# Kernel tuning notes

Measured on AMD Instinct MI355X. Metric: run time of the kernel, lower is better.

Reference implementation:

```python
import jax, jax.numpy as jnp
import numpy as np

B = 512
N_ENT = 100000
N_REL = 64
D = 200          # embed_dim
D1 = 10          # embed_shape (emb_dim1)
D2 = 20          # embed_dim // embed_shape (emb_dim2)
K = 3            # kernel_size
C = 32           # out_channels
FC_IN = C * (2 * D1 - K + 1) * (D2 - K + 1)  # 32*18*18 = 10368
EPS = 1e-5       # BatchNorm eps
LS = 0.1         # label_smoothing
LAM = 1e-5       # kg_l2_loss_lambda


def setup_inputs() -> dict:
    key = jax.random.key(0)
    ks = jax.random.split(key, 8)
    return dict(
        entity_w=jax.random.normal(ks[0], (N_ENT, D), jnp.float32) * 0.1,
        relation_w=jax.random.normal(ks[1], (N_REL, D), jnp.float32) * 0.1,
        conv_w=jax.random.normal(ks[2], (C, 1, K, K), jnp.float32) * 0.1,
        conv_b=jnp.zeros((C,), jnp.float32),
        fc_w=jax.random.normal(ks[3], (D, FC_IN), jnp.float32) * 0.02,
        fc_b=jnp.zeros((D,), jnp.float32),
        b=jnp.zeros((N_ENT,), jnp.float32),
        bn0_g=jnp.ones((1,), jnp.float32), bn0_b=jnp.zeros((1,), jnp.float32),
        bn1_g=jnp.ones((C,), jnp.float32), bn1_b=jnp.zeros((C,), jnp.float32),
        bn2_g=jnp.ones((D,), jnp.float32), bn2_b=jnp.zeros((D,), jnp.float32),
        h=jax.random.randint(ks[4], (B,), 0, N_ENT),
        r=jax.random.randint(ks[5], (B,), 0, N_REL),
        pos_t=jax.random.randint(ks[6], (B,), 0, N_ENT),
    )


def _bn(x, g, b, axes, shape):
    # training-mode batchnorm (batch statistics), biased variance as in torch
    m = jnp.mean(x, axes, keepdims=True)
    v = jnp.var(x, axes, keepdims=True)
    return (x - m) * jax.lax.rsqrt(v + EPS) * g.reshape(shape) + b.reshape(shape)


def _l2_mean(x):
    # torch: mean(sum(x**2, dim=1) / 2)
    return jnp.mean(jnp.sum(x * x, axis=1) / 2.0)


def reference(entity_w, relation_w, conv_w, conv_b, fc_w, fc_b, b,
              bn0_g, bn0_b, bn1_g, bn1_b, bn2_g, bn2_b, h, r, pos_t):
    h_e = entity_w[h].reshape(B, 1, D1, D2)
    r_e = relation_w[r].reshape(B, 1, D1, D2)
    x = jnp.concatenate([h_e, r_e], axis=2)           # [B,1,2*D1,D2]
    x = _bn(x, bn0_g, bn0_b, (0, 2, 3), (1, 1, 1, 1))
    x = jax.lax.conv_general_dilated(
        x, conv_w, (1, 1), 'VALID',
        dimension_numbers=('NCHW', 'OIHW', 'NCHW')) + conv_b.reshape(1, C, 1, 1)
    x = _bn(x, bn1_g, bn1_b, (0, 2, 3), (1, C, 1, 1))
    x = jax.nn.relu(x).reshape(B, -1)                 # [B, FC_IN]
    x = x @ fc_w.T + fc_b                             # [B, D]
    x = _bn(x, bn2_g, bn2_b, (0,), (1, D))
    x = jax.nn.leaky_relu(x)                          # slope 0.01 = torch default
    scores = x @ entity_w.T + b                       # [B, N_ENT]
    # BCEWithLogits with smoothed label y = (1-LS)*onehot(pos_t) + 1/N_ENT,
    # loss = mean(softplus(s) - s*y); one-hot never materialized.
    sp_sum = jnp.sum(jax.nn.softplus(scores))
    xy_sum = jnp.sum(scores) / N_ENT + (1.0 - LS) * jnp.sum(
        scores[jnp.arange(B), pos_t])
    kg_loss = (sp_sum - xy_sum) / (B * N_ENT)
    l2 = _l2_mean(h_e) + _l2_mean(r_e) + _l2_mean(conv_w) + _l2_mean(fc_w)
    return kg_loss + LAM * l2
```

## Files before the change

kernel.cpp:

```cpp
#include <hip/hip_runtime.h>
#include <math.h>

#define NB_B 512
#define NE 100000
#define NE_PAD 100032
#define DD 200
#define CC 32
#define FCIN 10368
#define HW 324
#define BNEPS 1e-5f
#define KP 224

#define ENT2_BLKS 3126
#define FCW_BLKS 1013
#define GATH_OFF2 (ENT2_BLKS + FCW_BLKS)

typedef __attribute__((ext_vector_type(8))) short short8;
typedef __attribute__((ext_vector_type(4))) float floatx4;


static __device__ __forceinline__ float blk_reduce(float v, volatile float* sbuf) {
  for (int o = 32; o > 0; o >>= 1) v += __shfl_down(v, o, 64);
  int lane = threadIdx.x & 63, wid = threadIdx.x >> 6;
  if (lane == 0) sbuf[wid] = v;
  __syncthreads();
  float r = 0.f;
  int nw = (blockDim.x + 63) >> 6;
  if ((int)threadIdx.x < nw) r = sbuf[threadIdx.x];
  if (threadIdx.x < 64) {
    for (int o = 32; o > 0; o >>= 1) r += __shfl_down(r, o, 64);
  }
  __syncthreads();
  return r;
}

static __device__ __forceinline__ unsigned short f32_to_bf16(float f) {
  unsigned int u = __float_as_uint(f);
  u += 0x7fffu + ((u >> 16) & 1u);
  return (unsigned short)(u >> 16);
}
static __device__ __forceinline__ float bf16_to_f32(unsigned short b) {
  return __uint_as_float(((unsigned int)b) << 16);
}

__global__ __launch_bounds__(256) void k_cvt(const float* __restrict__ ent,
                                             unsigned short* __restrict__ entb,
                                             const float* __restrict__ fcw,
                                             unsigned short* __restrict__ fcwb,
                                             const float* __restrict__ rel,
                                             const int* __restrict__ h,
                                             const int* __restrict__ r,
                                             float* __restrict__ x0,
                                             double* dacc) {
  __shared__ float xs[6432];
  int t = threadIdx.x;
  if (blockIdx.x < ENT2_BLKS) {
    int tile = blockIdx.x;
    for (int g = t; g < 1600; g += 256) {
      int rr = g / 50, c4 = g - rr * 50;
      int row = tile * 32 + rr;
      float4 u = {0.f, 0.f, 0.f, 0.f};
      if (row < NE) u = *(const float4*)(ent + (long)row * DD + c4 * 4);
      float* p = &xs[rr * 201 + c4 * 4];
      p[0] = u.x; p[1] = u.y; p[2] = u.z; p[3] = u.w;
    }
    __syncthreads();
    unsigned short* dst = entb + (long)tile * 7168;
    for (int g = t; g < 896; g += 256) {
      int c = g >> 5, rr = g & 31;
      short8 o = (short8){0, 0, 0, 0, 0, 0, 0, 0};
      if (c < 25) {
        const float* p = &xs[rr * 201 + c * 8];
        o[0] = (short)f32_to_bf16(p[0]); o[1] = (short)f32_to_bf16(p[1]);
        o[2] = (short)f32_to_bf16(p[2]); o[3] = (short)f32_to_bf16(p[3]);
        o[4] = (short)f32_to_bf16(p[4]); o[5] = (short)f32_to_bf16(p[5]);
        o[6] = (short)f32_to_bf16(p[6]); o[7] = (short)f32_to_bf16(p[7]);
      }
      *(short8*)(dst + g * 8) = o;
    }
  } else if (blockIdx.x < GATH_OFF2) {
    int g = (blockIdx.x - ENT2_BLKS) * 256 + t;
    float sq = 0.f;
    if (g < 259200) {
      const float4* s = (const float4*)(fcw + (long)g * 8);
      float4 u = s[0], v = s[1];
      sq = u.x*u.x + u.y*u.y + u.z*u.z + u.w*u.w
         + v.x*v.x + v.y*v.y + v.z*v.z + v.w*v.w;
      ushort4 o0, o1;
      o0.x = f32_to_bf16(u.x); o0.y = f32_to_bf16(u.y);
      o0.z = f32_to_bf16(u.z); o0.w = f32_to_bf16(u.w);
      o1.x = f32_to_bf16(v.x); o1.y = f32_to_bf16(v.y);
      o1.z = f32_to_bf16(v.z); o1.w = f32_to_bf16(v.w);
      ushort4* d = (ushort4*)(fcwb + (long)g * 8);
      d[0] = o0; d[1] = o1;
    }
    float tq = blk_reduce(sq, xs);
    if (t == 0) atomicAdd(&dacc[67], (double)tq);
  } else {
    int b = blockIdx.x - GATH_OFF2;
    int hi = h[b], ri = r[b];
    float s = 0.f, sq = 0.f;
    for (int i = t; i < 400; i += 256) {
      float v = (i < 200) ? ent[(long)hi * DD + i] : rel[(long)ri * DD + (i - 200)];
      x0[b * 400 + i] = v;
      s += v; sq += v * v;
    }
    float ts = blk_reduce(s, xs);
    float tq = blk_reduce(sq, xs);
    if (t == 0) {
      atomicAdd(&dacc[0], (double)ts);
      atomicAdd(&dacc[1], (double)tq);
    }
  }
}

__global__ __launch_bounds__(256) void k_conv(const float* __restrict__ x0,
                       const float* __restrict__ convw, const float* __restrict__ convb,
                       const float* __restrict__ g0, const float* __restrict__ b0,
                       unsigned short* __restrict__ yb, double* dacc) {
  __shared__ float xs[400], wsm[288], cbs[32], ssum[32], ssq[32];
  __shared__ float a0s, s0s;
  int b = blockIdx.x, t = threadIdx.x;
  for (int i = t; i < 400; i += 256) xs[i] = x0[b * 400 + i];
  for (int i = t; i < 288; i += 256) wsm[i] = convw[i];
  if (t < 32) cbs[t] = convb[t];
  if (t == 0) {
    double m = dacc[0] / 204800.0;
    double v = dacc[1] / 204800.0 - m * m;
    float a = g0[0] * rsqrtf((float)v + BNEPS);
    a0s = a; s0s = b0[0] - (float)m * a;
  }
  __syncthreads();
  float a0 = a0s, s0 = s0s;
  for (int i = t; i < 400; i += 256) xs[i] = a0 * xs[i] + s0;
  __syncthreads();
  int c = t >> 3, sub = t & 7;
  const float* w = &wsm[c * 9];
  float cb = cbs[c];
  float s = 0.f, sq = 0.f;
  for (int e = sub; e < HW; e += 8) {
    int oh = e / 18, ow = e - oh * 18;
    const float* xp = &xs[oh * 20 + ow];
    float acc = cb
       + xp[0] * w[0] + xp[1] * w[1] + xp[2] * w[2]
       + xp[20] * w[3] + xp[21] * w[4] + xp[22] * w[5]
       + xp[40] * w[6] + xp[41] * w[7] + xp[42] * w[8];
    yb[(long)b * FCIN + c * HW + e] = f32_to_bf16(acc);
    s += acc; sq += acc * acc;
  }
  s += __shfl_xor(s, 1, 64); sq += __shfl_xor(sq, 1, 64);
  s += __shfl_xor(s, 2, 64); sq += __shfl_xor(sq, 2, 64);
  s += __shfl_xor(s, 4, 64); sq += __shfl_xor(sq, 4, 64);
  if (sub == 0) { ssum[c] = s; ssq[c] = sq; }
  __syncthreads();
  if (t < 32) {
    atomicAdd(&dacc[2 + t], (double)ssum[t]);
    atomicAdd(&dacc[34 + t], (double)ssq[t]);
  }
}

__global__ __launch_bounds__(256) void k_prep(unsigned short* __restrict__ yb,
                                              const float* __restrict__ g1,
                                              const float* __restrict__ b1,
                                              const double* __restrict__ dacc) {
  __shared__ float a1s[32], sh1s[32];
  int t = threadIdx.x;
  if (t < 32) {
    double cnt = 512.0 * 324.0;
    double m = dacc[2 + t] / cnt, v = dacc[34 + t] / cnt - m * m;
    float a = g1[t] * rsqrtf((float)v + BNEPS);
    a1s[t] = a; sh1s[t] = b1[t] - (float)m * a;
  }
  __syncthreads();
  int g = blockIdx.x * 256 + t;
  int row = g / 1296;
  int c8 = (g - row * 1296) * 8;
  unsigned short* p = yb + (long)row * FCIN + c8;
  ushort4 v0 = ((ushort4*)p)[0], v1 = ((ushort4*)p)[1];
  unsigned short e[8] = {v0.x, v0.y, v0.z, v0.w, v1.x, v1.y, v1.z, v1.w};
#pragma unroll
  for (int j = 0; j < 8; j++) {
    int c = (c8 + j) / HW;
    float f = a1s[c] * bf16_to_f32(e[j]) + sh1s[c];
    e[j] = f32_to_bf16(fmaxf(f, 0.f));
  }
  v0.x = e[0]; v0.y = e[1]; v0.z = e[2]; v0.w = e[3];
  v1.x = e[4]; v1.y = e[5]; v1.z = e[6]; v1.w = e[7];
  ((ushort4*)p)[0] = v0; ((ushort4*)p)[1] = v1;
}

__global__ __launch_bounds__(64) void k_fc3(const unsigned short* __restrict__ yb,
                                            const unsigned short* __restrict__ fcwb,
                                            float* __restrict__ Cp) {
  int wid = blockIdx.x;
  int ks = wid >> 5, rem = wid & 31;
  int mt = rem >> 2, nt = rem & 3;
  int m0 = mt * 64, n0 = nt * 64;
  int lane = threadIdx.x;
  int quad = lane >> 4, lr = lane & 15;
  long kbeg = (long)ks * 864;

  const unsigned short* arow[4];
  const unsigned short* brow[4];
#pragma unroll
  for (int mi = 0; mi < 4; mi++)
    arow[mi] = yb + (long)(m0 + mi * 16 + lr) * FCIN + kbeg + quad * 8;
#pragma unroll
  for (int ni = 0; ni < 4; ni++) {
    int d = n0 + ni * 16 + lr;
    if (d > DD - 1) d = DD - 1;
    brow[ni] = fcwb + (long)d * FCIN + kbeg + quad * 8;
  }

  floatx4 acc[4][4];
#pragma unroll
  for (int i = 0; i < 4; i++)
#pragma unroll
    for (int j = 0; j < 4; j++) acc[i][j] = (floatx4){0.f, 0.f, 0.f, 0.f};

  short8 sA[3][4], sB[3][4];
#pragma unroll
  for (int c = 0; c < 3; c++) {
#pragma unroll
    for (int mi = 0; mi < 4; mi++) sA[c][mi] = *(const short8*)(arow[mi] + c * 32);
#pragma unroll
    for (int ni = 0; ni < 4; ni++) sB[c][ni] = *(const short8*)(brow[ni] + c * 32);
  }
  for (int c3 = 0; c3 < 9; c3++) {
    int cc = c3 * 3;
#pragma unroll
    for (int j = 0; j < 3; j++) {
#pragma unroll
      for (int ni = 0; ni < 4; ni++)
#pragma unroll
        for (int mi = 0; mi < 4; mi++)
          acc[mi][ni] = __builtin_amdgcn_mfma_f32_16x16x32_bf16(sA[j][mi], sB[j][ni], acc[mi][ni], 0, 0, 0);
      int nxt = cc + j + 3;
      if (nxt < 27) {
#pragma unroll
        for (int mi = 0; mi < 4; mi++) sA[j][mi] = *(const short8*)(arow[mi] + nxt * 32);
#pragma unroll
        for (int ni = 0; ni < 4; ni++) sB[j][ni] = *(const short8*)(brow[ni] + nxt * 32);
      }
    }
  }

  float* out = Cp + (long)ks * (NB_B * DD);
#pragma unroll
  for (int ni = 0; ni < 4; ni++) {
    int d = n0 + ni * 16 + lr;
    if (d < DD) {
#pragma unroll
      for (int mi = 0; mi < 4; mi++) {
        int mbase = m0 + mi * 16 + quad * 4;
#pragma unroll
        for (int rg = 0; rg < 4; rg++)
          out[(mbase + rg) * DD + d] = acc[mi][ni][rg];
      }
    }
  }
}

__global__ void k_fcbn(const float* __restrict__ Cp, const float* __restrict__ fcb,
                       const float* __restrict__ g2, const float* __restrict__ b2,
                       float* __restrict__ Cfc, float* __restrict__ a2,
                       float* __restrict__ b2c) {
  int d = blockIdx.x, lane = threadIdx.x;
  float fb = fcb[d];
  float s = 0.f, sq = 0.f;
  for (int b = lane; b < NB_B; b += 64) {
    float v = 0.f;
#pragma unroll
    for (int p = 0; p < 12; p++) v += Cp[(long)p * (NB_B * DD) + b * DD + d];
    Cfc[b * DD + d] = v;
    float w = v + fb;
    s += w; sq += w * w;
  }
  for (int o = 32; o > 0; o >>= 1) { s += __shfl_down(s, o, 64); sq += __shfl_down(sq, o, 64); }
  if (lane == 0) {
    float m = s / 512.f, v = sq / 512.f - m * m;
    float a = g2[d] * rsqrtf(v + BNEPS);
    a2[d] = a; b2c[d] = b2[d] - m * a;
  }
}

__global__ __launch_bounds__(256) void k_xfinal(const float* __restrict__ Cfc,
                         const float* __restrict__ fcb,
                         const float* __restrict__ a2, const float* __restrict__ b2c,
                         const float* __restrict__ ent, const float* __restrict__ bias,
                         const int* __restrict__ pos,
                         float* __restrict__ xf, unsigned short* __restrict__ xfb,
                         double* dacc) {
  __shared__ float xs[224];
  __shared__ float sbuf[8];
  int b = blockIdx.x, t = threadIdx.x;
  if (t < KP) {
    float xv = 0.f;
    if (t < DD) {
      float v = Cfc[b * DD + t] + fcb[t];
      xv = a2[t] * v + b2c[t];
      xv = xv >= 0.f ? xv : 0.01f * xv;
      xf[b * DD + t] = xv;
    }
    xfb[b * KP + t] = f32_to_bf16(xv);
    xs[t] = xv;
  }
  __syncthreads();
  int e = pos[b];
  float s = (t < DD) ? xs[t] * ent[(long)e * DD + t] : 0.f;
  float ts = blk_reduce(s, sbuf);
  if (t == 0) atomicAdd(&dacc[70], (double)(ts + bias[e]));
}

static __device__ __forceinline__ void sc_compute10(
    const unsigned short* __restrict__ buf, const float (&bv)[2],
    const short8 (&af)[2][7], int quad, int lr, float& sp, float& ss) {
#pragma unroll
  for (int ni = 0; ni < 2; ni++) {
    float b1v = bv[ni];
    floatx4 acc0 = (floatx4){0.f, 0.f, 0.f, 0.f};
    floatx4 acc1 = (floatx4){0.f, 0.f, 0.f, 0.f};
#pragma unroll
    for (int kc = 0; kc < 7; kc++) {
      int c = kc * 4 + quad;
      short8 bsv = *(const short8*)(buf + c * 256 + (ni * 16 + lr) * 8);
      acc0 = __builtin_amdgcn_mfma_f32_16x16x32_bf16(af[0][kc], bsv, acc0, 0, 0, 0);
      acc1 = __builtin_amdgcn_mfma_f32_16x16x32_bf16(af[1][kc], bsv, acc1, 0, 0, 0);
    }
#pragma unroll
    for (int rg2 = 0; rg2 < 4; rg2++) {
      float s1 = acc0[rg2] + b1v;
      ss += s1;
      float m1 = s1 * 1.4426950408889634f;
      float e2 = __builtin_amdgcn_exp2f(-__builtin_fabsf(m1));
      sp += fmaxf(m1, 0.f) + __builtin_amdgcn_logf(1.f + e2);
    }
#pragma unroll
    for (int rg2 = 0; rg2 < 4; rg2++) {
      float s1 = acc1[rg2] + b1v;
      ss += s1;
      float m1 = s1 * 1.4426950408889634f;
      float e2 = __builtin_amdgcn_exp2f(-__builtin_fabsf(m1));
      sp += fmaxf(m1, 0.f) + __builtin_amdgcn_logf(1.f + e2);
    }
  }
}

__global__ __launch_bounds__(512) void k_scores11(
    const unsigned short* __restrict__ entb,
    const unsigned short* __restrict__ xfb,
    const float* __restrict__ bias, double* dacc) {
  __shared__ unsigned short Bs[2][7168];
  __shared__ float sbuf[8];
  int t = threadIdx.x;
  int wv = t >> 6, lane = t & 63;
  int quad = lane >> 4, lr = lane & 15;
  int b = blockIdx.x;
  int rh = b & 1;
  int chunk = b >> 1;
  int nt = (chunk < 54) ? 7 : 6;
  int t0 = chunk * 6 + (chunk < 54 ? chunk : 54);

  short8 af[2][7];
#pragma unroll
  for (int mi = 0; mi < 2; mi++) {
    const unsigned short* ap =
        xfb + (size_t)(rh * 256 + wv * 32 + mi * 16 + lr) * KP + quad * 8;
#pragma unroll
    for (int kc = 0; kc < 7; kc++) af[mi][kc] = *(const short8*)(ap + kc * 32);
  }

#define STAGE11(bufp, tile)                                                    \
  {                                                                            \
    _Pragma("unroll")                                                          \
    for (int i_ = 0; i_ < 2; i_++) {                                           \
      int s_ = wv * 2 + i_;                                                    \
      if (s_ < 14) {                                                           \
        const unsigned short* gp_ =                                            \
            entb + (size_t)(tile) * 7168 + s_ * 512 + lane * 8;                \
        __builtin_amdgcn_global_load_lds(                                      \
            (const __attribute__((address_space(1))) unsigned int*)gp_,       \
            (__attribute__((address_space(3))) unsigned int*)((bufp) + s_ * 512), \
            16, 0, 0);                                                         \
      }                                                                        \
    }                                                                          \
  }

  float sp = 0.f, ss = 0.f;
  float bv[2], bvn[2];

  STAGE11(&Bs[0][0], t0);
#pragma unroll
  for (int ni = 0; ni < 2; ni++) {
    int e = t0 * 32 + ni * 16 + lr;
    bv[ni] = (e < NE) ? bias[e] : 0.f;
  }
  __syncthreads();

  int cur = 0;
#pragma unroll 1
  for (int i = 0; i < nt; i++) {
    if (i + 1 < nt) {
      STAGE11(&Bs[cur ^ 1][0], t0 + i + 1);
      int e0n = (t0 + i + 1) * 32 + lr;
      bvn[0] = (e0n < NE) ? bias[e0n] : 0.f;
      bvn[1] = (e0n + 16 < NE) ? bias[e0n + 16] : 0.f;
    }
    sc_compute10(&Bs[cur][0], bv, af, quad, lr, sp, ss);
    __syncthreads();
    bv[0] = bvn[0]; bv[1] = bvn[1];
    cur ^= 1;
  }
#undef STAGE11

  sp *= 0.6931471805599453f;
  float tsp = blk_reduce(sp, sbuf);
  float tss = blk_reduce(ss, sbuf);
  if (t == 0) {
    atomicAdd(&dacc[68], (double)tsp);
    atomicAdd(&dacc[69], (double)tss);
  }
}

__global__ void k_final(const float* __restrict__ convw, const double* dacc, float* out) {
  int t = threadIdx.x;
  float sq = 0.f;
  for (int i = t; i < 288; i += 64) { float w = convw[i]; sq += w * w; }
  for (int o = 32; o > 0; o >>= 1) sq += __shfl_down(sq, o, 64);
  if (t == 0) {
    double SP = dacc[68] - 16384.0 * 0.6931471805599453;
    double S2 = dacc[69], S3 = dacc[70];
    double xy = S2 / (double)NE + 0.9 * S3;
    double kg = (SP - xy) / ((double)NB_B * (double)NE);
    double l2 = dacc[1] / 204800.0 + (double)sq / 576.0 + dacc[67] / 400.0;
    out[0] = (float)(kg + 1e-5 * l2);
  }
}

extern "C" void kernel_launch(void* const* d_in, const int* in_sizes, int n_in,
                              void* d_out, int out_size, void* d_ws, size_t ws_size,
                              hipStream_t stream) {
  const float* ent   = (const float*)d_in[0];
  const float* rel   = (const float*)d_in[1];
  const float* convw = (const float*)d_in[2];
  const float* convb = (const float*)d_in[3];
  const float* fcw   = (const float*)d_in[4];
  const float* fcb   = (const float*)d_in[5];
  const float* bias  = (const float*)d_in[6];
  const float* g0    = (const float*)d_in[7];
  const float* b0    = (const float*)d_in[8];
  const float* g1    = (const float*)d_in[9];
  const float* b1    = (const float*)d_in[10];
  const float* g2    = (const float*)d_in[11];
  const float* b2    = (const float*)d_in[12];
  const int*   h     = (const int*)d_in[13];
  const int*   r     = (const int*)d_in[14];
  const int*   pos   = (const int*)d_in[15];

  char* ws = (char*)d_ws;
  double* dacc = (double*)(ws + 0);
  float* a2  = (float*)(ws + 16384 + 256);
  float* b2c = (float*)(ws + 16384 + 1056);
  float* x0  = (float*)(ws + 32768);
  float* Cfc = (float*)(ws + 851968);
  float* xf  = (float*)(ws + 1261568);
  unsigned short* yb   = (unsigned short*)(ws + 1671168);
  unsigned short* fcwb = (unsigned short*)(ws + 12288000);
  unsigned short* xfb  = (unsigned short*)(ws + 16435200);
  unsigned short* entb = (unsigned short*)(ws + 16664576);
  float* Cp = (float*)(ws + 61507584);

  hipMemsetAsync(dacc, 0, 8192, stream);

  k_cvt<<<GATH_OFF2 + 512, 256, 0, stream>>>(ent, entb, fcw, fcwb, rel, h, r, x0, dacc);
  k_conv<<<512, 256, 0, stream>>>(x0, convw, convb, g0, b0, yb, dacc);
  k_prep<<<2592, 256, 0, stream>>>(yb, g1, b1, dacc);
  k_fc3<<<384, 64, 0, stream>>>(yb, fcwb, Cp);
  k_fcbn<<<200, 64, 0, stream>>>(Cp, fcb, g2, b2, Cfc, a2, b2c);
  k_xfinal<<<512, 256, 0, stream>>>(Cfc, fcb, a2, b2c, ent, bias, pos, xf, xfb, dacc);
  k_scores11<<<1024, 512, 0, stream>>>(entb, xfb, bias, dacc);
  k_final<<<1, 64, 0, stream>>>(convw, dacc, (float*)d_out);
}
```

Baseline: 293.1 us.

## Split fused conversion kernel, widen fc-BN reduction, prioritize MFMA issue

Splits the combined conversion/gather kernel into three separate launches, so the small gather and fc_w kernels no longer need the large shared-memory allocation and can run at higher occupancy. Rewrites the fc batch-norm kernel to use 512 threads per block, one per batch row, with a block reduction instead of a 64-lane loop. Adds s_setprio around the MFMA loop in the scores kernel to favour matrix-instruction issue. The split adds two extra kernel launches and serialises stages that previously shared one grid.

```diff
diff --git a/kernel.cpp b/kernel.cpp
--- a/kernel.cpp
+++ b/kernel.cpp
@@ -13,7 +13,6 @@
 
 #define ENT2_BLKS 3126
 #define FCW_BLKS 1013
-#define GATH_OFF2 (ENT2_BLKS + FCW_BLKS)
 
 typedef __attribute__((ext_vector_type(8))) short short8;
 typedef __attribute__((ext_vector_type(4))) float floatx4;
@@ -43,74 +42,78 @@
   return __uint_as_float(((unsigned int)b) << 16);
 }
 
-__global__ __launch_bounds__(256) void k_cvt(const float* __restrict__ ent,
-                                             unsigned short* __restrict__ entb,
-                                             const float* __restrict__ fcw,
-                                             unsigned short* __restrict__ fcwb,
-                                             const float* __restrict__ rel,
-                                             const int* __restrict__ h,
-                                             const int* __restrict__ r,
-                                             float* __restrict__ x0,
-                                             double* dacc) {
+__global__ __launch_bounds__(256) void k_cvt_ent(const float* __restrict__ ent,
+                                                 unsigned short* __restrict__ entb) {
   __shared__ float xs[6432];
   int t = threadIdx.x;
-  if (blockIdx.x < ENT2_BLKS) {
-    int tile = blockIdx.x;
-    for (int g = t; g < 1600; g += 256) {
-      int rr = g / 50, c4 = g - rr * 50;
-      int row = tile * 32 + rr;
-      float4 u = {0.f, 0.f, 0.f, 0.f};
-      if (row < NE) u = *(const float4*)(ent + (long)row * DD + c4 * 4);
-      float* p = &xs[rr * 201 + c4 * 4];
-      p[0] = u.x; p[1] = u.y; p[2] = u.z; p[3] = u.w;
-    }
-    __syncthreads();
-    unsigned short* dst = entb + (long)tile * 7168;
-    for (int g = t; g < 896; g += 256) {
-      int c = g >> 5, rr = g & 31;
-      short8 o = (short8){0, 0, 0, 0, 0, 0, 0, 0};
-      if (c < 25) {
-        const float* p = &xs[rr * 201 + c * 8];
-        o[0] = (short)f32_to_bf16(p[0]); o[1] = (short)f32_to_bf16(p[1]);
-        o[2] = (short)f32_to_bf16(p[2]); o[3] = (short)f32_to_bf16(p[3]);
-        o[4] = (short)f32_to_bf16(p[4]); o[5] = (short)f32_to_bf16(p[5]);
-        o[6] = (short)f32_to_bf16(p[6]); o[7] = (short)f32_to_bf16(p[7]);
-      }
-      *(short8*)(dst + g * 8) = o;
-    }
-  } else if (blockIdx.x < GATH_OFF2) {
-    int g = (blockIdx.x - ENT2_BLKS) * 256 + t;
-    float sq = 0.f;
-    if (g < 259200) {
-      const float4* s = (const float4*)(fcw + (long)g * 8);
-      float4 u = s[0], v = s[1];
-      sq = u.x*u.x + u.y*u.y + u.z*u.z + u.w*u.w
-         + v.x*v.x + v.y*v.y + v.z*v.z + v.w*v.w;
-      ushort4 o0, o1;
-      o0.x = f32_to_bf16(u.x); o0.y = f32_to_bf16(u.y);
-      o0.z = f32_to_bf16(u.z); o0.w = f32_to_bf16(u.w);
-      o1.x = f32_to_bf16(v.x); o1.y = f32_to_bf16(v.y);
-      o1.z = f32_to_bf16(v.z); o1.w = f32_to_bf16(v.w);
-      ushort4* d = (ushort4*)(fcwb + (long)g * 8);
-      d[0] = o0; d[1] = o1;
-    }
-    float tq = blk_reduce(sq, xs);
-    if (t == 0) atomicAdd(&dacc[67], (double)tq);
-  } else {
-    int b = blockIdx.x - GATH_OFF2;
-    int hi = h[b], ri = r[b];
-    float s = 0.f, sq = 0.f;
-    for (int i = t; i < 400; i += 256) {
-      float v = (i < 200) ? ent[(long)hi * DD + i] : rel[(long)ri * DD + (i - 200)];
-      x0[b * 400 + i] = v;
-      s += v; sq += v * v;
-    }
-    float ts = blk_reduce(s, xs);
-    float tq = blk_reduce(sq, xs);
-    if (t == 0) {
-      atomicAdd(&dacc[0], (double)ts);
-      atomicAdd(&dacc[1], (double)tq);
-    }
+  int tile = blockIdx.x;
+  for (int g = t; g < 1600; g += 256) {
+    int rr = g / 50, c4 = g - rr * 50;
+    int row = tile * 32 + rr;
+    float4 u = {0.f, 0.f, 0.f, 0.f};
+    if (row < NE) u = *(const float4*)(ent + (long)row * DD + c4 * 4);
+    float* p = &xs[rr * 201 + c4 * 4];
+    p[0] = u.x; p[1] = u.y; p[2] = u.z; p[3] = u.w;
+  }
+  __syncthreads();
+  unsigned short* dst = entb + (long)tile * 7168;
+  for (int g = t; g < 896; g += 256) {
+    int c = g >> 5, rr = g & 31;
+    short8 o = (short8){0, 0, 0, 0, 0, 0, 0, 0};
+    if (c < 25) {
+      const float* p = &xs[rr * 201 + c * 8];
+      o[0] = (short)f32_to_bf16(p[0]); o[1] = (short)f32_to_bf16(p[1]);
+      o[2] = (short)f32_to_bf16(p[2]); o[3] = (short)f32_to_bf16(p[3]);
+      o[4] = (short)f32_to_bf16(p[4]); o[5] = (short)f32_to_bf16(p[5]);
+      o[6] = (short)f32_to_bf16(p[6]); o[7] = (short)f32_to_bf16(p[7]);
+    }
+    *(short8*)(dst + g * 8) = o;
+  }
+}
+
+__global__ __launch_bounds__(256) void k_cvt_fcw(const float* __restrict__ fcw,
+                                                 unsigned short* __restrict__ fcwb,
+                                                 double* dacc) {
+  __shared__ float sbuf[8];
+  int g = blockIdx.x * 256 + threadIdx.x;
+  float sq = 0.f;
+  if (g < 259200) {
+    const float4* s = (const float4*)(fcw + (long)g * 8);
+    float4 u = s[0], v = s[1];
+    sq = u.x*u.x + u.y*u.y + u.z*u.z + u.w*u.w
+       + v.x*v.x + v.y*v.y + v.z*v.z + v.w*v.w;
+    ushort4 o0, o1;
+    o0.x = f32_to_bf16(u.x); o0.y = f32_to_bf16(u.y);
+    o0.z = f32_to_bf16(u.z); o0.w = f32_to_bf16(u.w);
+    o1.x = f32_to_bf16(v.x); o1.y = f32_to_bf16(v.y);
+    o1.z = f32_to_bf16(v.z); o1.w = f32_to_bf16(v.w);
+    ushort4* d = (ushort4*)(fcwb + (long)g * 8);
+    d[0] = o0; d[1] = o1;
+  }
+  float tq = blk_reduce(sq, sbuf);
+  if (threadIdx.x == 0) atomicAdd(&dacc[67], (double)tq);
+}
+
+__global__ __launch_bounds__(256) void k_gather(const float* __restrict__ ent,
+                                                const float* __restrict__ rel,
+                                                const int* __restrict__ h,
+                                                const int* __restrict__ r,
+                                                float* __restrict__ x0,
+                                                double* dacc) {
+  __shared__ float sbuf[8];
+  int b = blockIdx.x, t = threadIdx.x;
+  int hi = h[b], ri = r[b];
+  float s = 0.f, sq = 0.f;
+  for (int i = t; i < 400; i += 256) {
+    float v = (i < 200) ? ent[(long)hi * DD + i] : rel[(long)ri * DD + (i - 200)];
+    x0[b * 400 + i] = v;
+    s += v; sq += v * v;
+  }
+  float ts = blk_reduce(s, sbuf);
+  float tq = blk_reduce(sq, sbuf);
+  if (t == 0) {
+    atomicAdd(&dacc[0], (double)ts);
+    atomicAdd(&dacc[1], (double)tq);
   }
 }
 
@@ -261,25 +264,24 @@
   }
 }
 
-__global__ void k_fcbn(const float* __restrict__ Cp, const float* __restrict__ fcb,
+__global__ __launch_bounds__(512) void k_fcbn(const float* __restrict__ Cp,
+                       const float* __restrict__ fcb,
                        const float* __restrict__ g2, const float* __restrict__ b2,
                        float* __restrict__ Cfc, float* __restrict__ a2,
                        float* __restrict__ b2c) {
-  int d = blockIdx.x, lane = threadIdx.x;
+  __shared__ float sbuf[8];
+  int d = blockIdx.x, b = threadIdx.x;
   float fb = fcb[d];
-  float s = 0.f, sq = 0.f;
-  for (int b = lane; b < NB_B; b += 64) {
-    float v = 0.f;
-#pragma unroll
-    for (int p = 0; p < 12; p++) v += Cp[(long)p * (NB_B * DD) + b * DD + d];
-    Cfc[b * DD + d] = v;
-    float w = v + fb;
-    s += w; sq += w * w;
-  }
-  for (int o = 32; o > 0; o >>= 1) { s += __shfl_down(s, o, 64); sq += __shfl_down(sq, o, 64); }
-  if (lane == 0) {
-    float m = s / 512.f, v = sq / 512.f - m * m;
-    float a = g2[d] * rsqrtf(v + BNEPS);
+  float v = 0.f;
+#pragma unroll
+  for (int p = 0; p < 12; p++) v += Cp[(long)p * (NB_B * DD) + b * DD + d];
+  Cfc[b * DD + d] = v;
+  float w = v + fb;
+  float s = blk_reduce(w, sbuf);
+  float sq = blk_reduce(w * w, sbuf);
+  if (b == 0) {
+    float m = s / 512.f, vv = sq / 512.f - m * m;
+    float a = g2[d] * rsqrtf(vv + BNEPS);
     a2[d] = a; b2c[d] = b2[d] - m * a;
   }
 }
@@ -320,6 +322,7 @@
     float b1v = bv[ni];
     floatx4 acc0 = (floatx4){0.f, 0.f, 0.f, 0.f};
     floatx4 acc1 = (floatx4){0.f, 0.f, 0.f, 0.f};
+    __builtin_amdgcn_s_setprio(1);
 #pragma unroll
     for (int kc = 0; kc < 7; kc++) {
       int c = kc * 4 + quad;
@@ -327,6 +330,7 @@
       acc0 = __builtin_amdgcn_mfma_f32_16x16x32_bf16(af[0][kc], bsv, acc0, 0, 0, 0);
       acc1 = __builtin_amdgcn_mfma_f32_16x16x32_bf16(af[1][kc], bsv, acc1, 0, 0, 0);
     }
+    __builtin_amdgcn_s_setprio(0);
 #pragma unroll
     for (int rg2 = 0; rg2 < 4; rg2++) {
       float s1 = acc0[rg2] + b1v;
@@ -472,11 +476,13 @@
 
   hipMemsetAsync(dacc, 0, 8192, stream);
 
-  k_cvt<<<GATH_OFF2 + 512, 256, 0, stream>>>(ent, entb, fcw, fcwb, rel, h, r, x0, dacc);
+  k_gather<<<512, 256, 0, stream>>>(ent, rel, h, r, x0, dacc);
+  k_cvt_fcw<<<FCW_BLKS, 256, 0, stream>>>(fcw, fcwb, dacc);
+  k_cvt_ent<<<ENT2_BLKS, 256, 0, stream>>>(ent, entb);
   k_conv<<<512, 256, 0, stream>>>(x0, convw, convb, g0, b0, yb, dacc);
   k_prep<<<2592, 256, 0, stream>>>(yb, g1, b1, dacc);
   k_fc3<<<384, 64, 0, stream>>>(yb, fcwb, Cp);
-  k_fcbn<<<200, 64, 0, stream>>>(Cp, fcb, g2, b2, Cfc, a2, b2c);
+  k_fcbn<<<200, 512, 0, stream>>>(Cp, fcb, g2, b2, Cfc, a2, b2c);
   k_xfinal<<<512, 256, 0, stream>>>(Cfc, fcb, a2, b2c, ent, bias, pos, xf, xfb, dacc);
   k_scores11<<<1024, 512, 0, stream>>>(entb, xfb, bias, dacc);
   k_final<<<1, 64, 0, stream>>>(convw, dacc, (float*)d_out);
```

Result: slower. 312.3 us (+6.6%).
